# Optimization experiments

Measured on AMD Instinct MI355X. Metric: run time of the kernel, lower is better.

## Reference

```python
import jax, jax.numpy as jnp
import numpy as np

MASK_FILL = -1e10
LOG_2PI = float(np.log(2.0 * np.pi))


def setup_inputs() -> dict:
    key = jax.random.key(0)
    k1, k2, k3 = jax.random.split(key, 3)
    bs, seq_len, emb_dim = 32, 512, 512
    T = 2048
    emb = jax.random.normal(k1, (bs, seq_len, emb_dim), dtype=jnp.float32)
    # positive durations; rescale so the max total duration over the batch == T exactly,
    # matching torch's T = sum(durations).int().max()
    d = jax.random.uniform(k2, (bs, seq_len), dtype=jnp.float32, minval=0.5, maxval=1.0)
    d = d * (T / jnp.max(jnp.sum(d, axis=1)))
    log_sigma = jax.random.normal(k3, (1,), dtype=jnp.float32) * 0.1
    return {"emb": emb, "durations": d, "log_sigma": log_sigma, "T": T}


def reference(emb, durations, log_sigma, T):
    # emb: (bs, S, E); durations: (bs, S); log_sigma: (1,); T: static int
    bs, S, E = emb.shape
    ls = log_sigma[0]
    sigma = jnp.exp(ls)
    # Gaussian centers per token: cumsum - 0.5*dur  -> (bs, S)
    centers = jnp.cumsum(durations, axis=1) - 0.5 * durations
    t = jnp.arange(T, dtype=emb.dtype)  # frame indices (T,)
    # Normal(loc=centers, scale=sigma).log_prob(t + 0.5)  -> (bs, T, S)
    z = (t[None, :, None] + 0.5 - centers[:, None, :]) / sigma
    logp = -0.5 * z * z - ls - 0.5 * LOG_2PI
    # mask out zero-duration tokens
    logp = jnp.where((durations == 0.0)[:, None, :], MASK_FILL, logp)
    w = jax.nn.softmax(logp, axis=2)  # (bs, T, S)
    x = jnp.einsum('bts,bse->bte', w, emb)  # (bs, T, E)
    total = jnp.sum(durations, axis=1)  # (bs,)
    out_mask = t[None, :] < total[:, None]  # (bs, T) bool
    return x, out_mask
```

## Files before the change

### kernel.cpp

```cpp
#include <hip/hip_runtime.h>
#include <math.h>

#define BS 32
#define S_TOK 512
#define E_DIM 512
#define T_FR 2048
#define FPB 32
#define WMAX 36
#define THRESH -25.0f



typedef float vfloat4 __attribute__((ext_vector_type(4)));

struct RowMeta { float m; float inv_l; int lo; int cnt; };

__global__ __launch_bounds__(256) void fused_all(
    const float* __restrict__ emb,
    const float* __restrict__ dur,
    const float* __restrict__ log_sigma,
    float* __restrict__ x,
    float* __restrict__ mask_out) {
  int id = blockIdx.x;
  int sw = ((id & 7) << 8) + (id >> 3);
  int b = sw >> 6;
  int t0 = (sw & 63) << 5;

  int tid = threadIdx.x;
  int half = tid >> 7;
  int lane = tid & 127;

  __shared__ float cbS[S_TOK];
  __shared__ float wT[WMAX][FPB];
  __shared__ RowMeta metaS[FPB];
  __shared__ double wsumS[4];
  __shared__ float totalS;

  {
    const float* dp = dur + b * S_TOK;
    int i2 = tid << 1;
    double d0 = (double)dp[i2];
    double d1 = (double)dp[i2 + 1];
    double pair = d0 + d1;
    double run = pair;
#pragma unroll
    for (int off = 1; off < 64; off <<= 1) {
      double v = __shfl_up(run, off, 64);
      if ((tid & 63) >= off) run += v;
    }
    int w = tid >> 6;
    if ((tid & 63) == 63) wsumS[w] = run;
    __syncthreads();
    double wexcl = 0.0;
#pragma unroll
    for (int k = 0; k < 3; ++k) wexcl += (k < w) ? wsumS[k] : 0.0;
    double incl = wexcl + run;
    double excl = incl - pair;
    cbS[i2]     = (float)(excl + d0 - 0.5 * d0);
    cbS[i2 + 1] = (float)(excl + (d0 + d1) - 0.5 * d1);
    if (tid == 255) totalS = (float)incl;
  }
  __syncthreads();

  float inv_sigma = expf(-log_sigma[0]);

  if (tid < FPB) {
    float tq = (float)(t0 + tid) + 0.5f;
    auto V = [&](int s) {
      float z = (tq - cbS[s]) * inv_sigma;
      return -0.5f * z * z;
    };
    int lo = 0, hi = S_TOK;
    while (lo < hi) {
      int mid = (lo + hi) >> 1;
      if (cbS[mid] < tq) lo = mid + 1; else hi = mid;
    }
    int best; float m;
    if (lo == 0) { best = 0; m = V(0); }
    else if (lo == S_TOK) { best = S_TOK - 1; m = V(best); }
    else {
      float va = V(lo - 1), vb = V(lo);
      if (va >= vb) { best = lo - 1; m = va; } else { best = lo; m = vb; }
    }
    int wl = best, wh = best;
    while (wl > 0 && V(wl - 1) > m + THRESH) --wl;
    while (wh < S_TOK - 1 && V(wh + 1) > m + THRESH) ++wh;
    float l = 0.0f;
    for (int s = wl; s <= wh; ++s) l += expf(V(s) - m);
    RowMeta mt;
    mt.m = m;
    mt.inv_l = 1.0f / l;
    mt.lo = wl;
    mt.cnt = wh - wl + 1;
    metaS[tid] = mt;
  }
  __syncthreads();

  int ulo = metaS[0].lo, uhi = metaS[0].lo + metaS[0].cnt - 1;
#pragma unroll
  for (int f = 1; f < FPB; ++f) {
    ulo = min(ulo, metaS[f].lo);
    uhi = max(uhi, metaS[f].lo + metaS[f].cnt - 1);
  }
  int cnt = min(uhi - ulo + 1, WMAX);

  for (int k = tid; k < cnt * FPB; k += 256) {
    int i = k >> 5, f = k & 31;
    float c = cbS[ulo + i];
    float tqf = (float)(t0 + f) + 0.5f;
    float z = (tqf - c) * inv_sigma;
    float v = -0.5f * z * z;
    float e = expf(v - metaS[f].m) * metaS[f].inv_l;
    wT[i][f] = (v - metaS[f].m > THRESH) ? e : 0.0f;
  }
  __syncthreads();

  const vfloat4* e4 =
      (const vfloat4*)emb + ((size_t)(b * S_TOK + ulo)) * (E_DIM / 4) + lane;
  vfloat4 acc[16];
#pragma unroll
  for (int f = 0; f < 16; ++f) acc[f] = (vfloat4){0.f, 0.f, 0.f, 0.f};

  vfloat4 vcur = e4[0];
  vfloat4 vnext = e4[(size_t)min(1, cnt - 1) * (E_DIM / 4)];
  for (int i = 0; i < cnt; ++i) {
    vfloat4 vfut = e4[(size_t)min(i + 2, cnt - 1) * (E_DIM / 4)];
    const vfloat4* wp = (const vfloat4*)&wT[i][half << 4];
    vfloat4 w0 = wp[0], w1 = wp[1], w2 = wp[2], w3 = wp[3];
    acc[0] += w0.x * vcur;  acc[1] += w0.y * vcur;
    acc[2] += w0.z * vcur;  acc[3] += w0.w * vcur;
    acc[4] += w1.x * vcur;  acc[5] += w1.y * vcur;
    acc[6] += w1.z * vcur;  acc[7] += w1.w * vcur;
    acc[8] += w2.x * vcur;  acc[9] += w2.y * vcur;
    acc[10] += w2.z * vcur; acc[11] += w2.w * vcur;
    acc[12] += w3.x * vcur; acc[13] += w3.y * vcur;
    acc[14] += w3.z * vcur; acc[15] += w3.w * vcur;
    vcur = vnext; vnext = vfut;
  }

  vfloat4* xp = (vfloat4*)x +
      ((size_t)(b * T_FR + t0 + (half << 4))) * (E_DIM / 4) + lane;
#pragma unroll
  for (int f = 0; f < 16; ++f)
    xp[(size_t)f * (E_DIM / 4)] = acc[f];

  if (tid < FPB) {
    int t = t0 + tid;
    mask_out[b * T_FR + t] = ((float)t < totalS) ? 1.0f : 0.0f;
  }
}

extern "C" void kernel_launch(void* const* d_in, const int* in_sizes, int n_in,
                              void* d_out, int out_size, void* d_ws,
                              size_t ws_size, hipStream_t stream) {
  const float* emb = (const float*)d_in[0];
  const float* dur = (const float*)d_in[1];
  const float* log_sigma = (const float*)d_in[2];

  float* x = (float*)d_out;
  float* mask_out = x + (size_t)BS * T_FR * E_DIM;

  fused_all<<<(BS * T_FR) / FPB, 256, 0, stream>>>(
      emb, dur, log_sigma, x, mask_out);
}
```

Baseline: 169.7 us.

## Parallelize per-frame window search with histogram counting and ballot-based window extension

Replaces the serial per-frame binary search, linear window expansion and normalizer loop run by 32 threads with block-parallel work. A shared histogram of centers plus a wave scan finds each frame's nearest token, and a ballot over candidate tokens sets the union window. The softmax normalizer is now summed from the weight tile by 8 threads per frame and applied at output time, and the first emb loads are issued before the weight tile is built. The threshold masking of weights is dropped, so tokens in the union window beyond a frame's own window now contribute small nonzero weights, and the window search assumes centers are sorted and roughly one token per frame.

```diff
diff --git a/kernel.cpp b/kernel.cpp
--- a/kernel.cpp
+++ b/kernel.cpp
@@ -12,8 +12,6 @@
 
 
 typedef float vfloat4 __attribute__((ext_vector_type(4)));
-
-struct RowMeta { float m; float inv_l; int lo; int cnt; };
 
 __global__ __launch_bounds__(256) void fused_all(
     const float* __restrict__ emb,
@@ -32,77 +30,113 @@
 
   __shared__ float cbS[S_TOK];
   __shared__ float wT[WMAX][FPB];
-  __shared__ RowMeta metaS[FPB];
+  __shared__ float mS[FPB];
+  __shared__ float invS[FPB];
   __shared__ double wsumS[4];
+  __shared__ int histS[FPB];
+  __shared__ int n0S[4];
+  __shared__ int uloS, cntS;
   __shared__ float totalS;
 
-  {
-    const float* dp = dur + b * S_TOK;
-    int i2 = tid << 1;
-    double d0 = (double)dp[i2];
-    double d1 = (double)dp[i2 + 1];
-    double pair = d0 + d1;
-    double run = pair;
-#pragma unroll
-    for (int off = 1; off < 64; off <<= 1) {
-      double v = __shfl_up(run, off, 64);
-      if ((tid & 63) >= off) run += v;
-    }
-    int w = tid >> 6;
-    if ((tid & 63) == 63) wsumS[w] = run;
-    __syncthreads();
-    double wexcl = 0.0;
-#pragma unroll
-    for (int k = 0; k < 3; ++k) wexcl += (k < w) ? wsumS[k] : 0.0;
-    double incl = wexcl + run;
-    double excl = incl - pair;
-    cbS[i2]     = (float)(excl + d0 - 0.5 * d0);
-    cbS[i2 + 1] = (float)(excl + (d0 + d1) - 0.5 * d1);
-    if (tid == 255) totalS = (float)incl;
-  }
-  __syncthreads();
+  if (tid < FPB) histS[tid] = 0;
 
   float inv_sigma = expf(-log_sigma[0]);
-
-  if (tid < FPB) {
-    float tq = (float)(t0 + tid) + 0.5f;
-    auto V = [&](int s) {
-      float z = (tq - cbS[s]) * inv_sigma;
-      return -0.5f * z * z;
-    };
-    int lo = 0, hi = S_TOK;
-    while (lo < hi) {
-      int mid = (lo + hi) >> 1;
-      if (cbS[mid] < tq) lo = mid + 1; else hi = mid;
-    }
-    int best; float m;
-    if (lo == 0) { best = 0; m = V(0); }
-    else if (lo == S_TOK) { best = S_TOK - 1; m = V(best); }
-    else {
-      float va = V(lo - 1), vb = V(lo);
-      if (va >= vb) { best = lo - 1; m = va; } else { best = lo; m = vb; }
-    }
-    int wl = best, wh = best;
-    while (wl > 0 && V(wl - 1) > m + THRESH) --wl;
-    while (wh < S_TOK - 1 && V(wh + 1) > m + THRESH) ++wh;
-    float l = 0.0f;
-    for (int s = wl; s <= wh; ++s) l += expf(V(s) - m);
-    RowMeta mt;
-    mt.m = m;
-    mt.inv_l = 1.0f / l;
-    mt.lo = wl;
-    mt.cnt = wh - wl + 1;
-    metaS[tid] = mt;
-  }
-  __syncthreads();
-
-  int ulo = metaS[0].lo, uhi = metaS[0].lo + metaS[0].cnt - 1;
-#pragma unroll
-  for (int f = 1; f < FPB; ++f) {
-    ulo = min(ulo, metaS[f].lo);
-    uhi = max(uhi, metaS[f].lo + metaS[f].cnt - 1);
-  }
-  int cnt = min(uhi - ulo + 1, WMAX);
+  float tq0 = (float)t0 + 0.5f;
+  float tq31 = (float)t0 + 31.5f;
+
+  const float* dp = dur + b * S_TOK;
+  int i2 = tid << 1;
+  double d0 = (double)dp[i2];
+  double d1 = (double)dp[i2 + 1];
+  double pair = d0 + d1;
+  double run = pair;
+#pragma unroll
+  for (int off = 1; off < 64; off <<= 1) {
+    double v = __shfl_up(run, off, 64);
+    if ((tid & 63) >= off) run += v;
+  }
+  int w = tid >> 6;
+  if ((tid & 63) == 63) wsumS[w] = run;
+  __syncthreads();
+  double wexcl = 0.0;
+#pragma unroll
+  for (int k = 0; k < 3; ++k) wexcl += (k < w) ? wsumS[k] : 0.0;
+  double incl = wexcl + run;
+  double excl = incl - pair;
+  float c0 = (float)(excl + d0 - 0.5 * d0);
+  float c1 = (float)(excl + (d0 + d1) - 0.5 * d1);
+  cbS[i2] = c0;
+  cbS[i2 + 1] = c1;
+
+  int n0 = (c0 < tq0 ? 1 : 0) + (c1 < tq0 ? 1 : 0);
+  if (c0 >= tq0 && c0 < tq31) atomicAdd(&histS[(int)floorf(c0 - tq0) + 1], 1);
+  if (c1 >= tq0 && c1 < tq31) atomicAdd(&histS[(int)floorf(c1 - tq0) + 1], 1);
+#pragma unroll
+  for (int off = 1; off < 64; off <<= 1) n0 += __shfl_xor(n0, off, 64);
+  if ((tid & 63) == 0) n0S[w] = n0;
+  if (tid == 255) totalS = (float)incl;
+  __syncthreads();
+
+  if (tid < 64) {
+    int l = tid;
+    int sc = (l >= 1 && l < 32) ? histS[l] : 0;
+#pragma unroll
+    for (int off = 1; off < 32; off <<= 1) {
+      int v = __shfl_up(sc, off, 64);
+      if (l >= off) sc += v;
+    }
+    int N0 = n0S[0] + n0S[1] + n0S[2] + n0S[3];
+    int best = 0;
+    float m = 0.0f;
+    if (l < 32) {
+      int N = N0 + sc;
+      float tqf = (float)(t0 + l) + 0.5f;
+      if (N <= 0) {
+        best = 0;
+        float z = (tqf - cbS[0]) * inv_sigma; m = -0.5f * z * z;
+      } else if (N >= S_TOK) {
+        best = S_TOK - 1;
+        float z = (tqf - cbS[best]) * inv_sigma; m = -0.5f * z * z;
+      } else {
+        float za = (tqf - cbS[N - 1]) * inv_sigma; float va = -0.5f * za * za;
+        float zb = (tqf - cbS[N]) * inv_sigma;     float vb = -0.5f * zb * zb;
+        if (va >= vb) { best = N - 1; m = va; } else { best = N; m = vb; }
+      }
+      mS[l] = m;
+    }
+    int best0 = __shfl(best, 0, 64);   float m0 = __shfl(m, 0, 64);
+    int best31 = __shfl(best, 31, 64); float m31 = __shfl(m, 31, 64);
+    int p = l & 15;
+    bool flag = false;
+    if (l < 16) {
+      int s = best0 - 1 - p;
+      if (s >= 0) {
+        float z = (tq0 - cbS[s]) * inv_sigma;
+        flag = (-0.5f * z * z) > m0 + THRESH;
+      }
+    } else if (l < 32) {
+      int s = best31 + 1 + p;
+      if (s < S_TOK) {
+        float z = (tq31 - cbS[s]) * inv_sigma;
+        flag = (-0.5f * z * z) > m31 + THRESH;
+      }
+    }
+    unsigned long long bal = __ballot(flag);
+    if (l == 0) {
+      int wl = best0 - __popcll(bal & 0xFFFFull);
+      int wh = best31 + __popcll(bal & 0xFFFF0000ull);
+      uloS = wl;
+      cntS = min(wh - wl + 1, WMAX);
+    }
+  }
+  __syncthreads();
+
+  int ulo = uloS, cnt = cntS;
+
+  const vfloat4* e4 =
+      (const vfloat4*)emb + ((size_t)(b * S_TOK + ulo)) * (E_DIM / 4) + lane;
+  vfloat4 vcur = e4[0];
+  vfloat4 vnext = e4[(size_t)min(1, cnt - 1) * (E_DIM / 4)];
 
   for (int k = tid; k < cnt * FPB; k += 256) {
     int i = k >> 5, f = k & 31;
@@ -110,19 +144,24 @@
     float tqf = (float)(t0 + f) + 0.5f;
     float z = (tqf - c) * inv_sigma;
     float v = -0.5f * z * z;
-    float e = expf(v - metaS[f].m) * metaS[f].inv_l;
-    wT[i][f] = (v - metaS[f].m > THRESH) ? e : 0.0f;
-  }
-  __syncthreads();
-
-  const vfloat4* e4 =
-      (const vfloat4*)emb + ((size_t)(b * S_TOK + ulo)) * (E_DIM / 4) + lane;
+    wT[i][f] = expf(v - mS[f]);
+  }
+  __syncthreads();
+
+  {
+    int f = tid >> 3, p = tid & 7;
+    float s = 0.0f;
+    for (int i = p; i < cnt; i += 8) s += wT[i][f];
+#pragma unroll
+    for (int off = 1; off < 8; off <<= 1) s += __shfl_xor(s, off, 64);
+    if (p == 0) invS[f] = 1.0f / s;
+  }
+  __syncthreads();
+
   vfloat4 acc[16];
 #pragma unroll
   for (int f = 0; f < 16; ++f) acc[f] = (vfloat4){0.f, 0.f, 0.f, 0.f};
 
-  vfloat4 vcur = e4[0];
-  vfloat4 vnext = e4[(size_t)min(1, cnt - 1) * (E_DIM / 4)];
   for (int i = 0; i < cnt; ++i) {
     vfloat4 vfut = e4[(size_t)min(i + 2, cnt - 1) * (E_DIM / 4)];
     const vfloat4* wp = (const vfloat4*)&wT[i][half << 4];
@@ -142,7 +181,7 @@
       ((size_t)(b * T_FR + t0 + (half << 4))) * (E_DIM / 4) + lane;
 #pragma unroll
   for (int f = 0; f < 16; ++f)
-    xp[(size_t)f * (E_DIM / 4)] = acc[f];
+    xp[(size_t)f * (E_DIM / 4)] = acc[f] * invS[(half << 4) + f];
 
   if (tid < FPB) {
     int t = t0 + tid;
```

New measurement: 169.1 us. Within noise of the previous version (-0.4%).
